# Performance work log

Measured on AMD Instinct MI355X. Metric: run time of the kernel, lower is better.

The kernel has to match this reference:

```python
import jax, jax.numpy as jnp
import numpy as np

T, B, IN, HID = 1024, 64, 512, 512


def setup_inputs() -> dict:
    key = jax.random.key(0)
    k1, k2, k3 = jax.random.split(key, 3)
    stdv = 1.0 / np.sqrt(HID)
    return {
        "inputs": jax.random.normal(k1, (T, B, IN), dtype=jnp.float32),
        "W_x": jax.random.uniform(k2, (4, HID, IN), jnp.float32, -stdv, stdv),
        "W_h": jax.random.uniform(k3, (4, HID, HID), jnp.float32, -stdv, stdv),
        "bias": jnp.zeros((4, HID), jnp.float32),
        "thresholds": jnp.zeros((HID, 8), jnp.float32),
        "h0": jnp.zeros((B, HID), jnp.float32),
        "c0": jnp.zeros((B, HID), jnp.float32),
    }


def unit_step(x):
    # forward of UnitStepFunction: 1.0 where x >= 0 else 0.0
    return (x >= 0).astype(x.dtype)


def reference(inputs, W_x, W_h, bias, thresholds, h0, c0):
    # Threshold-based weight masking (gate order: i, f, o, c).
    thr_x = thresholds[:, :4].T[:, :, None]   # (4, HID, 1)
    thr_h = thresholds[:, 4:].T[:, :, None]   # (4, HID, 1)
    mask_x = unit_step(jnp.abs(W_x) - thr_x)
    mask_h = unit_step(jnp.abs(W_h) - thr_h)
    Wx = jnp.swapaxes(W_x * mask_x, 1, 2)     # (4, IN, HID), pre-transposed
    Wh = jnp.swapaxes(W_h * mask_h, 1, 2)     # (4, HID, HID)

    def step(carry, X):
        H, C = carry
        # g: (4, B, HID) = X@W_x[g] + H@W_h[g] + b[g] for each gate
        g = (jnp.einsum('bi,gih->gbh', X, Wx)
             + jnp.einsum('bh,ghk->gbk', H, Wh)
             + bias[:, None, :])
        I = jax.nn.sigmoid(g[0])
        F = jax.nn.sigmoid(g[1])
        O = jax.nn.sigmoid(g[2])
        C_tilda = jnp.tanh(g[3])
        C = F * C + I * C_tilda
        H = O * jnp.tanh(C)
        return (H, C), H

    (_, _), outputs = jax.lax.scan(step, (h0, c0), inputs)
    return outputs  # (T, B, HID)
```

## Files before the change

### kernel.cpp

```cpp
#include <hip/hip_runtime.h>

#define TT 1024
#define BB 64
#define IN_ 512
#define HID_ 512
#define KTOT 1024
#define SLICE (BB * HID_)

#define AGENT __HIP_MEMORY_SCOPE_AGENT

typedef float v2f __attribute__((ext_vector_type(2)));

__device__ __forceinline__ float sigmoid_fast(float x) {
  return 1.0f / (1.0f + __expf(-x));
}

__device__ __forceinline__ float tanh_fast(float x) {
  float ax = fabsf(x);
  float e = __expf(2.0f * ax);
  float r = 1.0f - 2.0f / (e + 1.0f);
  return copysignf(r, x);
}

__device__ __forceinline__ float ld_llc(const float* p) {
  return __hip_atomic_load(const_cast<float*>(p), __ATOMIC_RELAXED, AGENT);
}
__device__ __forceinline__ void st_llc(float* p, float v) {
  __hip_atomic_store(p, v, __ATOMIC_RELAXED, AGENT);
}

__device__ __forceinline__ void gridbar(unsigned* ctr, unsigned target) {
  __syncthreads();
  if (threadIdx.x == 0) {
    __hip_atomic_fetch_add(ctr, 1u, __ATOMIC_RELAXED, AGENT);
    while (__hip_atomic_load(ctr, __ATOMIC_RELAXED, AGENT) < target)
      __builtin_amdgcn_s_sleep(2);
  }
  __syncthreads();
}

__global__ void prep_weights(const float* __restrict__ Wx,
                             const float* __restrict__ Wh,
                             const float* __restrict__ thr,
                             float* __restrict__ W4, unsigned* __restrict__ ctr) {
  if (blockIdx.x == 0 && threadIdx.x == 0) *ctr = 0;
  int idx = blockIdx.x * 256 + threadIdx.x;
  int k = idx >> 9;
  int j = idx & 511;
  float4 w4;
  float* wp = reinterpret_cast<float*>(&w4);
#pragma unroll
  for (int g = 0; g < 4; ++g) {
    float w, th;
    if (k < IN_) {
      w = Wx[(g * HID_ + j) * IN_ + k];
      th = thr[j * 8 + g];
    } else {
      w = Wh[(g * HID_ + j) * HID_ + (k - IN_)];
      th = thr[j * 8 + 4 + g];
    }
    float m = ((fabsf(w) - th) >= 0.0f) ? 1.0f : 0.0f;
    wp[g] = w * m;
  }
  reinterpret_cast<float4*>(W4)[idx] = w4;
}

__global__ void transpose_x(const float* __restrict__ X,
                            float* __restrict__ out,
                            float* __restrict__ xlast) {
  __shared__ float tile[64][129];
  int t = blockIdx.x >> 2;
  int k0 = (blockIdx.x & 3) * 128;
  const float* src = X + (size_t)t * (BB * IN_) + k0;
#pragma unroll
  for (int j = 0; j < 8; ++j) {
    int f = threadIdx.x + j * 256;
    int b = f >> 5;
    int m = (f & 31) * 4;
    float4 v = *reinterpret_cast<const float4*>(src + b * IN_ + m);
    tile[b][m + 0] = v.x; tile[b][m + 1] = v.y;
    tile[b][m + 2] = v.z; tile[b][m + 3] = v.w;
  }
  __syncthreads();
  float* dst = (t < TT - 1) ? (out + (size_t)(t + 1) * SLICE) : xlast;
  int b = threadIdx.x & 63;
  int ks = threadIdx.x >> 6;
#pragma unroll
  for (int u = 0; u < 32; ++u) {
    int kk = ks * 32 + u;
    dst[(k0 + kk) * BB + b] = tile[b][kk];
  }
}

__global__ void __launch_bounds__(512) lstm_rec(
    const float* __restrict__ W4, const float* __restrict__ bias,
    const float* __restrict__ h0p, const float* __restrict__ c0p,
    float* __restrict__ Hb0, float* __restrict__ Hb1,
    const float* __restrict__ xlast, float* __restrict__ out,
    unsigned* __restrict__ ctr) {
  __shared__ float wlds[KTOT * 8];
  __shared__ float red[8][64][9];
  const int tid = threadIdx.x;
  const int blk = blockIdx.x;
  const int b = tid & 63;
  const int ksub = __builtin_amdgcn_readfirstlane(tid >> 6);
  const int h0c = blk * 2;
  unsigned bar_target = 256;

  const float4* Wsrc = reinterpret_cast<const float4*>(W4);
  float4* Wdst = reinterpret_cast<float4*>(wlds);
  for (int i = tid; i < KTOT * 2; i += 512) {
    int k = i >> 1, r = i & 1;
    Wdst[k * 2 + r] = Wsrc[(k << 9) + h0c + r];
  }

  float C = 0.0f;
  if (tid < 128) {
    int hh = h0c + (tid >> 6);
    st_llc(&Hb0[hh * BB + b], h0p[b * HID_ + hh]);
    C = c0p[b * HID_ + hh];
  }
  gridbar(ctr, bar_target); bar_target += 256;

  for (int t = 0; t < TT; ++t) {
    const float* Hprev = (t & 1) ? Hb1 : Hb0;
    float* Hnext = (t & 1) ? Hb0 : Hb1;
    const float* Xs = (t < TT - 1) ? (out + (size_t)(t + 1) * SLICE) : xlast;
    const int k0 = ksub * 128;
    const float* wp = wlds + k0 * 8;

    v2f acc0 = {0.f, 0.f};
    v2f acc1 = {0.f, 0.f};
    v2f acc2 = {0.f, 0.f};
    v2f acc3 = {0.f, 0.f};
    if (ksub < 4) {
      const float* Abase = Xs + k0 * BB + b;
#pragma unroll 8
      for (int i = 0; i < 128; ++i) {
        float a = Abase[i * BB];
        float4 wa = *reinterpret_cast<const float4*>(wp + i * 8);
        float4 wb = *reinterpret_cast<const float4*>(wp + i * 8 + 4);
        v2f av = {a, a};
        acc0 = __builtin_elementwise_fma((v2f){wa.x, wa.y}, av, acc0);
        acc1 = __builtin_elementwise_fma((v2f){wa.z, wa.w}, av, acc1);
        acc2 = __builtin_elementwise_fma((v2f){wb.x, wb.y}, av, acc2);
        acc3 = __builtin_elementwise_fma((v2f){wb.z, wb.w}, av, acc3);
      }
    } else {
      const float* Abase = Hprev + (k0 - IN_) * BB + b;
#pragma unroll 8
      for (int i = 0; i < 128; ++i) {
        float a = ld_llc(Abase + i * BB);
        float4 wa = *reinterpret_cast<const float4*>(wp + i * 8);
        float4 wb = *reinterpret_cast<const float4*>(wp + i * 8 + 4);
        v2f av = {a, a};
        acc0 = __builtin_elementwise_fma((v2f){wa.x, wa.y}, av, acc0);
        acc1 = __builtin_elementwise_fma((v2f){wa.z, wa.w}, av, acc1);
        acc2 = __builtin_elementwise_fma((v2f){wb.x, wb.y}, av, acc2);
        acc3 = __builtin_elementwise_fma((v2f){wb.z, wb.w}, av, acc3);
      }
    }
    float* rp = &red[ksub][b][0];
    rp[0] = acc0.x; rp[1] = acc0.y; rp[2] = acc1.x; rp[3] = acc1.y;
    rp[4] = acc2.x; rp[5] = acc2.y; rp[6] = acc3.x; rp[7] = acc3.y;
    __syncthreads();

    if (tid < 128) {
      int hsub = tid >> 6;
      int hh = h0c + hsub;
      float gs[4];
#pragma unroll
      for (int gg = 0; gg < 4; ++gg) {
        float s = bias[gg * HID_ + hh];
#pragma unroll
        for (int ks = 0; ks < 8; ++ks) s += red[ks][b][hsub * 4 + gg];
        gs[gg] = s;
      }
      float I = sigmoid_fast(gs[0]);
      float F = sigmoid_fast(gs[1]);
      float O = sigmoid_fast(gs[2]);
      float Ctl = tanh_fast(gs[3]);
      C = F * C + I * Ctl;
      float H = O * tanh_fast(C);
      out[(size_t)t * SLICE + b * HID_ + hh] = H;
      st_llc(&Hnext[hh * BB + b], H);
    }
    gridbar(ctr, bar_target); bar_target += 256;
  }
}

extern "C" void kernel_launch(void* const* d_in, const int* in_sizes, int n_in,
                              void* d_out, int out_size, void* d_ws, size_t ws_size,
                              hipStream_t stream) {
  (void)in_sizes; (void)n_in; (void)out_size; (void)ws_size;
  const float* X    = (const float*)d_in[0];
  const float* Wx   = (const float*)d_in[1];
  const float* Wh   = (const float*)d_in[2];
  const float* bias = (const float*)d_in[3];
  const float* thr  = (const float*)d_in[4];
  const float* h0p  = (const float*)d_in[5];
  const float* c0p  = (const float*)d_in[6];
  float* out = (float*)d_out;

  float* W4 = (float*)d_ws;
  float* Hb0 = W4 + (size_t)KTOT * HID_ * 4;
  float* Hb1 = Hb0 + SLICE;
  float* xlast = Hb1 + SLICE;
  unsigned* ctr = (unsigned*)(xlast + SLICE);

  prep_weights<<<(KTOT * HID_) / 256, 256, 0, stream>>>(Wx, Wh, thr, W4, ctr);
  transpose_x<<<TT * 4, 256, 0, stream>>>(X, out, xlast);

  void* args[] = {&W4, &bias, &h0p, &c0p, &Hb0, &Hb1, &xlast, &out, &ctr};
  hipLaunchCooperativeKernel(reinterpret_cast<void*>(lstm_rec),
                             dim3(256), dim3(512), args, 0, stream);
}
```

Measured before the change: 11.23 ms.

## Register-tile recurrent GEMV over batch and reduce partials with cross-lane permlane swaps

Each thread now computes 8 batch columns times 8 gate outputs over a 16-wide K slice, instead of one batch column over 128 K. This raises reuse of each weight and activation load: activations are read as float4 or 64-bit atomic loads, and weights come from a swizzled LDS layout that avoids bank conflicts. The partial sums across the K lanes of a wave are combined with v_permlane32/16 swaps and a shuffle before a smaller LDS reduction. Bias is hoisted into registers. The 64-value register tile raises register pressure, which may hurt occupancy despite the launch_bounds(512,2) hint, and the added shuffle work lengthens each recurrent step.

```diff
diff --git a/kernel.cpp b/kernel.cpp
--- a/kernel.cpp
+++ b/kernel.cpp
@@ -25,6 +25,9 @@
 __device__ __forceinline__ float ld_llc(const float* p) {
   return __hip_atomic_load(const_cast<float*>(p), __ATOMIC_RELAXED, AGENT);
 }
+__device__ __forceinline__ unsigned long long ld_llc64(const unsigned long long* p) {
+  return __hip_atomic_load(const_cast<unsigned long long*>(p), __ATOMIC_RELAXED, AGENT);
+}
 __device__ __forceinline__ void st_llc(float* p, float v) {
   __hip_atomic_store(p, v, __ATOMIC_RELAXED, AGENT);
 }
@@ -37,6 +40,15 @@
       __builtin_amdgcn_s_sleep(2);
   }
   __syncthreads();
+}
+
+__device__ __forceinline__ float plswap32_sum(float a, float b) {
+  asm("v_permlane32_swap_b32 %0, %1" : "+v"(a), "+v"(b));
+  return a + b;
+}
+__device__ __forceinline__ float plswap16_sum(float a, float b) {
+  asm("v_permlane16_swap_b32 %0, %1" : "+v"(a), "+v"(b));
+  return a + b;
 }
 
 __global__ void prep_weights(const float* __restrict__ Wx,
@@ -92,89 +104,153 @@
   }
 }
 
-__global__ void __launch_bounds__(512) lstm_rec(
+__global__ void __launch_bounds__(512, 2) lstm_rec(
     const float* __restrict__ W4, const float* __restrict__ bias,
     const float* __restrict__ h0p, const float* __restrict__ c0p,
     float* __restrict__ Hb0, float* __restrict__ Hb1,
     const float* __restrict__ xlast, float* __restrict__ out,
     unsigned* __restrict__ ctr) {
   __shared__ float wlds[KTOT * 8];
-  __shared__ float red[8][64][9];
+  __shared__ float red3[8 * 8 * 72];
   const int tid = threadIdx.x;
   const int blk = blockIdx.x;
-  const int b = tid & 63;
-  const int ksub = __builtin_amdgcn_readfirstlane(tid >> 6);
+  const int wv = __builtin_amdgcn_readfirstlane(tid >> 6);
+  const int lane = tid & 63;
+  const int ks = tid >> 3;
+  const int bt = tid & 7;
   const int h0c = blk * 2;
   unsigned bar_target = 256;
 
-  const float4* Wsrc = reinterpret_cast<const float4*>(W4);
-  float4* Wdst = reinterpret_cast<float4*>(wlds);
-  for (int i = tid; i < KTOT * 2; i += 512) {
-    int k = i >> 1, r = i & 1;
-    Wdst[k * 2 + r] = Wsrc[(k << 9) + h0c + r];
+  {
+    const float4* Wsrc = reinterpret_cast<const float4*>(W4);
+    float4* Wdst = reinterpret_cast<float4*>(wlds);
+    for (int i = tid; i < KTOT * 2; i += 512) {
+      int k = i >> 1, r = i & 1;
+      int swz = (((k >> 4) & 3) << 1) | ((k >> 6) & 1);
+      Wdst[((k * 2) + r) ^ swz] = Wsrc[(k << 9) + h0c + r];
+    }
   }
 
   float C = 0.0f;
+  float bias_r[4] = {0.f, 0.f, 0.f, 0.f};
   if (tid < 128) {
     int hh = h0c + (tid >> 6);
+    int b = tid & 63;
     st_llc(&Hb0[hh * BB + b], h0p[b * HID_ + hh]);
     C = c0p[b * HID_ + hh];
+#pragma unroll
+    for (int g = 0; g < 4; ++g) bias_r[g] = bias[g * HID_ + hh];
   }
   gridbar(ctr, bar_target); bar_target += 256;
+
+  const int swz = ((ks & 3) << 1) | ((ks >> 2) & 1);
+  const float4* wbase = reinterpret_cast<const float4*>(wlds) + ks * 32;
 
   for (int t = 0; t < TT; ++t) {
     const float* Hprev = (t & 1) ? Hb1 : Hb0;
     float* Hnext = (t & 1) ? Hb0 : Hb1;
     const float* Xs = (t < TT - 1) ? (out + (size_t)(t + 1) * SLICE) : xlast;
-    const int k0 = ksub * 128;
-    const float* wp = wlds + k0 * 8;
-
-    v2f acc0 = {0.f, 0.f};
-    v2f acc1 = {0.f, 0.f};
-    v2f acc2 = {0.f, 0.f};
-    v2f acc3 = {0.f, 0.f};
-    if (ksub < 4) {
-      const float* Abase = Xs + k0 * BB + b;
-#pragma unroll 8
-      for (int i = 0; i < 128; ++i) {
-        float a = Abase[i * BB];
-        float4 wa = *reinterpret_cast<const float4*>(wp + i * 8);
-        float4 wb = *reinterpret_cast<const float4*>(wp + i * 8 + 4);
-        v2f av = {a, a};
-        acc0 = __builtin_elementwise_fma((v2f){wa.x, wa.y}, av, acc0);
-        acc1 = __builtin_elementwise_fma((v2f){wa.z, wa.w}, av, acc1);
-        acc2 = __builtin_elementwise_fma((v2f){wb.x, wb.y}, av, acc2);
-        acc3 = __builtin_elementwise_fma((v2f){wb.z, wb.w}, av, acc3);
+
+    v2f acc[2][4][4];
+#pragma unroll
+    for (int h = 0; h < 2; ++h)
+#pragma unroll
+      for (int g = 0; g < 4; ++g)
+#pragma unroll
+        for (int p = 0; p < 4; ++p) acc[h][g][p] = (v2f){0.f, 0.f};
+
+    if (wv < 4) {
+      const float4* Ax = reinterpret_cast<const float4*>(Xs) + ks * 256 + bt * 2;
+#pragma unroll 4
+      for (int j = 0; j < 16; ++j) {
+        float4 a0 = Ax[j * 16];
+        float4 a1 = Ax[j * 16 + 1];
+        float4 wa = wbase[(j * 2) ^ swz];
+        float4 wb = wbase[(j * 2 + 1) ^ swz];
+        v2f av[4] = {{a0.x, a0.y}, {a0.z, a0.w}, {a1.x, a1.y}, {a1.z, a1.w}};
+        const float wg[2][4] = {{wa.x, wa.y, wa.z, wa.w},
+                                {wb.x, wb.y, wb.z, wb.w}};
+#pragma unroll
+        for (int h = 0; h < 2; ++h)
+#pragma unroll
+          for (int g = 0; g < 4; ++g) {
+            v2f wvv = {wg[h][g], wg[h][g]};
+#pragma unroll
+            for (int p = 0; p < 4; ++p)
+              acc[h][g][p] = __builtin_elementwise_fma(wvv, av[p], acc[h][g][p]);
+          }
       }
     } else {
-      const float* Abase = Hprev + (k0 - IN_) * BB + b;
-#pragma unroll 8
-      for (int i = 0; i < 128; ++i) {
-        float a = ld_llc(Abase + i * BB);
-        float4 wa = *reinterpret_cast<const float4*>(wp + i * 8);
-        float4 wb = *reinterpret_cast<const float4*>(wp + i * 8 + 4);
-        v2f av = {a, a};
-        acc0 = __builtin_elementwise_fma((v2f){wa.x, wa.y}, av, acc0);
-        acc1 = __builtin_elementwise_fma((v2f){wa.z, wa.w}, av, acc1);
-        acc2 = __builtin_elementwise_fma((v2f){wb.x, wb.y}, av, acc2);
-        acc3 = __builtin_elementwise_fma((v2f){wb.z, wb.w}, av, acc3);
-      }
-    }
-    float* rp = &red[ksub][b][0];
-    rp[0] = acc0.x; rp[1] = acc0.y; rp[2] = acc1.x; rp[3] = acc1.y;
-    rp[4] = acc2.x; rp[5] = acc2.y; rp[6] = acc3.x; rp[7] = acc3.y;
+      const unsigned long long* Ah =
+          reinterpret_cast<const unsigned long long*>(Hprev) +
+          (ks * 16 - IN_) * 32 + bt * 4;
+#pragma unroll 4
+      for (int j = 0; j < 16; ++j) {
+        unsigned long long q0 = ld_llc64(Ah + j * 32 + 0);
+        unsigned long long q1 = ld_llc64(Ah + j * 32 + 1);
+        unsigned long long q2 = ld_llc64(Ah + j * 32 + 2);
+        unsigned long long q3 = ld_llc64(Ah + j * 32 + 3);
+        float4 wa = wbase[(j * 2) ^ swz];
+        float4 wb = wbase[(j * 2 + 1) ^ swz];
+        v2f av[4] = {__builtin_bit_cast(v2f, q0), __builtin_bit_cast(v2f, q1),
+                     __builtin_bit_cast(v2f, q2), __builtin_bit_cast(v2f, q3)};
+        const float wg[2][4] = {{wa.x, wa.y, wa.z, wa.w},
+                                {wb.x, wb.y, wb.z, wb.w}};
+#pragma unroll
+        for (int h = 0; h < 2; ++h)
+#pragma unroll
+          for (int g = 0; g < 4; ++g) {
+            v2f wvv = {wg[h][g], wg[h][g]};
+#pragma unroll
+            for (int p = 0; p < 4; ++p)
+              acc[h][g][p] = __builtin_elementwise_fma(wvv, av[p], acc[h][g][p]);
+          }
+      }
+    }
+
+    float vals[64];
+#pragma unroll
+    for (int h = 0; h < 2; ++h)
+#pragma unroll
+      for (int g = 0; g < 4; ++g)
+#pragma unroll
+        for (int p = 0; p < 4; ++p) {
+          vals[(h * 4 + g) * 8 + p * 2]     = acc[h][g][p].x;
+          vals[(h * 4 + g) * 8 + p * 2 + 1] = acc[h][g][p].y;
+        }
+#pragma unroll
+    for (int r = 0; r < 32; ++r) vals[r] = plswap32_sum(vals[r], vals[r + 32]);
+#pragma unroll
+    for (int r = 0; r < 16; ++r) vals[r] = plswap16_sum(vals[r], vals[r + 16]);
+    {
+      const bool hi = (lane & 8) != 0;
+#pragma unroll
+      for (int r = 0; r < 8; ++r) {
+        float keep = hi ? vals[r + 8] : vals[r];
+        float send = hi ? vals[r] : vals[r + 8];
+        vals[r] = keep + __shfl_xor(send, 8, 64);
+      }
+    }
+    {
+      int hgo = (lane >> 3) & 7;
+      float* rp = &red3[(wv * 8 + hgo) * 72 + bt * 9];
+#pragma unroll
+      for (int i = 0; i < 8; ++i) rp[i] = vals[i];
+    }
     __syncthreads();
 
     if (tid < 128) {
       int hsub = tid >> 6;
       int hh = h0c + hsub;
+      int b = tid & 63;
+      int boff = (b >> 3) * 9 + (b & 7);
       float gs[4];
 #pragma unroll
-      for (int gg = 0; gg < 4; ++gg) {
-        float s = bias[gg * HID_ + hh];
-#pragma unroll
-        for (int ks = 0; ks < 8; ++ks) s += red[ks][b][hsub * 4 + gg];
-        gs[gg] = s;
+      for (int g = 0; g < 4; ++g) {
+        float s = bias_r[g];
+#pragma unroll
+        for (int w = 0; w < 8; ++w) s += red3[(w * 8 + hsub * 4 + g) * 72 + boff];
+        gs[g] = s;
       }
       float I = sigmoid_fast(gs[0]);
       float F = sigmoid_fast(gs[1]);
```

Result: slower. 14.05 ms (+25.1%).
